# Performance work log

Hardware: AMD Instinct MI355X
Metric: run time of the kernel (lower is better)

The kernel has to match this reference:

```python
import jax, jax.numpy as jnp
import numpy as np

B, N_EX, N_KC, D_E, D_C, D_H = 32, 1024, 128, 64, 64, 64


def setup_inputs() -> dict:
    key = jax.random.key(0)
    ks = jax.random.split(key, 20)
    return {
        "h": jax.random.normal(ks[0], (B, N_KC, D_H), jnp.float32),
        "ex": jax.random.uniform(ks[1], (B, N_EX), jnp.float32),
        "su": jax.random.uniform(ks[2], (B,), jnp.float32),
        "ex_graph": jax.random.uniform(ks[3], (N_EX, N_KC), jnp.float32),
        "kc_gamma": jax.random.normal(ks[4], (N_KC, N_KC), jnp.float32),
        "W_ex": jax.random.normal(ks[5], (D_E, 2 * N_EX), jnp.float32) * 0.02,
        "W_kc": jax.random.normal(ks[6], (D_C, N_KC), jnp.float32) * 0.05,
        "tgru_wih": jax.random.normal(ks[7], (3 * D_H, D_E), jnp.float32) * 0.05,
        "tgru_whh": jax.random.normal(ks[8], (3 * D_H, D_H), jnp.float32) * 0.05,
        "tgru_bih": jax.random.normal(ks[9], (3 * D_H,), jnp.float32) * 0.05,
        "tgru_bhh": jax.random.normal(ks[10], (3 * D_H,), jnp.float32) * 0.05,
        "fpart_w": jax.random.normal(ks[11], (D_H, D_C + D_H), jnp.float32) * 0.05,
        "fpart_b": jax.random.normal(ks[12], (D_H,), jnp.float32) * 0.05,
        "ulin_w": jax.random.normal(ks[13], (D_H, D_H), jnp.float32) * 0.05,
        "ulin_b": jax.random.normal(ks[14], (D_H,), jnp.float32) * 0.05,
        "ugru_wih": jax.random.normal(ks[15], (3 * D_H, D_H), jnp.float32) * 0.05,
        "ugru_whh": jax.random.normal(ks[16], (3 * D_H, D_H), jnp.float32) * 0.05,
        "ugru_bih": jax.random.normal(ks[17], (3 * D_H,), jnp.float32) * 0.05,
        "ugru_bhh": jax.random.normal(ks[18], (3 * D_H,), jnp.float32) * 0.05,
    }


def _gru_cell(x, h, wih, whh, bih, bhh):
    # torch.nn.GRUCell: gates in order r, z, n
    gi = x @ wih.T + bih
    gh = h @ whh.T + bhh
    ir, iz, inn = jnp.split(gi, 3, axis=-1)
    hr, hz, hn = jnp.split(gh, 3, axis=-1)
    r = jax.nn.sigmoid(ir + hr)
    z = jax.nn.sigmoid(iz + hz)
    n = jnp.tanh(inn + r * hn)
    return (1.0 - z) * n + z * h


def reference(h, ex, su, ex_graph, kc_gamma, W_ex, W_kc,
              tgru_wih, tgru_whh, tgru_bih, tgru_bhh,
              fpart_w, fpart_b, ulin_w, ulin_b,
              ugru_wih, ugru_whh, ugru_bih, ugru_bhh):
    bsz, n_kc, d_h = h.shape
    kc_graph = jax.nn.sigmoid(kc_gamma)  # (n_kc, n_kc)

    # exercise embedding from [ex*su, ex*(1-su)]
    x_id = jnp.concatenate([ex * su[:, None], ex * (1.0 - su)[:, None]], axis=-1)  # (B, 2*n_ex)
    x = x_id @ W_ex.T  # (B, d_e)

    kci = ex @ ex_graph  # (B, n_kc)
    kci_flat = kci.reshape(bsz * n_kc, 1)

    # temporal GRU update, gated by kci
    x_rep = jnp.broadcast_to(x[:, None, :], (bsz, n_kc, x.shape[-1])).reshape(bsz * n_kc, -1)
    h_flat = h.reshape(bsz * n_kc, d_h)
    th = _gru_cell(x_rep, h_flat, tgru_wih, tgru_whh, tgru_bih, tgru_bhh)
    new_h = (1.0 - kci_flat) * h_flat + kci_flat * th  # (B*n_kc, d_h)

    delta_h = (new_h - h_flat).reshape(bsz, n_kc, d_h)

    # kc_embeddings(eye(n_kc)) == W_kc.T : (n_kc, d_c)
    e = W_kc.T
    # fpart(concat([delta_h_i, e_j])) split into the two weight blocks
    W_dh = fpart_w[:, :d_h]   # acts on delta_h
    W_e = fpart_w[:, d_h:]    # acts on e
    dpart = delta_h @ W_dh.T                      # (B, n_kc_i, d_h)
    epart = e @ W_e.T + fpart_b                   # (n_kc_j, d_h)
    pre = dpart[:, :, None, :] + epart[None, None, :, :]  # (B, i, j, d_h)
    partij = jax.nn.relu(pre)
    partij = partij * kc_graph[None, :, :, None] * kci[:, :, None, None]
    partj = jnp.sum(partij, axis=1)               # (B, n_kc_j, d_h)

    outj = jax.nn.relu(partj @ ulin_w.T + ulin_b).reshape(bsz * n_kc, d_h)
    kcj = (kci @ kc_graph).reshape(bsz * n_kc, 1)

    uh = _gru_cell(outj, new_h, ugru_wih, ugru_whh, ugru_bih, ugru_bhh)
    h_out = (1.0 - kcj) * new_h + kcj * uh
    return h_out.reshape(bsz, n_kc, d_h)
```

## Files before the change

### kernel.cpp

```cpp
#include <hip/hip_runtime.h>
#include <math.h>

#define NB  32
#define NKC 128
#define DH  64
#define NEX 1024
#define G3  192

#define XOFF    0
#define KCIOFF  2048
#define EPOFF   6144
#define NHOFF   14336
#define DPOFF   276480

__device__ __forceinline__ float sigf(float x) { return 1.0f / (1.0f + expf(-x)); }

__global__ __launch_bounds__(256) void k0_prep(
    const float* __restrict__ ex, const float* __restrict__ su,
    const float* __restrict__ ex_graph, const float* __restrict__ W_ex,
    const float* __restrict__ W_kc, const float* __restrict__ fpart_w,
    const float* __restrict__ fpart_b, float* __restrict__ ws)
{
    int t = threadIdx.x, wave = t >> 6, lane = t & 63;
    int blk = blockIdx.x;
    __shared__ float kred[256];
    __shared__ float fwT[64 * 65];
    __shared__ float wkS[64 * 33];

    if (blk < 256) {
        int b = blk >> 3;
        int dbase = (blk & 7) * 8;
        float sub = su[b];
        const float* exb = ex + (size_t)b * NEX;
        float er[16];
        #pragma unroll
        for (int i = 0; i < 16; ++i) er[i] = exb[lane + i * 64];
        #pragma unroll
        for (int p = 0; p < 2; ++p) {
            int d = dbase + wave * 2 + p;
            const float* wr = W_ex + (size_t)d * (2 * NEX);
            float a1 = 0.f, a2 = 0.f;
            #pragma unroll
            for (int i = 0; i < 16; ++i) {
                int k = lane + i * 64;
                a1 = fmaf(er[i], wr[k], a1);
                a2 = fmaf(er[i], wr[NEX + k], a2);
            }
            float v = sub * a1 + (1.0f - sub) * a2;
            #pragma unroll
            for (int off = 32; off; off >>= 1) v += __shfl_down(v, off, 64);
            if (lane == 0) ws[XOFF + b * DH + d] = v;
        }
    } else if (blk < 512) {
        int q = blk - 256;
        int b = q >> 3, i0 = (q & 7) * 16;
        int i = t & 15, ks = t >> 4;
        const float* exb = ex + (size_t)b * NEX;
        const float* eg = ex_graph + i0 + i;
        int kb = ks * 64;
        float a = 0.f;
        #pragma unroll 4
        for (int k = 0; k < 64; ++k)
            a = fmaf(exb[kb + k], eg[(size_t)(kb + k) * NKC], a);
        kred[t] = a;
        __syncthreads();
        if (t < 16) {
            float s = 0.f;
            #pragma unroll
            for (int r = 0; r < 16; ++r) s += kred[r * 16 + t];
            ws[KCIOFF + b * NKC + i0 + t] = s;
        }
    } else {
        int eb = blk - 512;
        for (int idx = t; idx < 4096; idx += 256) {
            int d = idx >> 6, c = idx & 63;
            fwT[c * 65 + d] = fpart_w[d * 128 + 64 + c];
        }
        for (int idx = t; idx < 2048; idx += 256) {
            int c = idx >> 5, jl = idx & 31;
            wkS[c * 33 + jl] = W_kc[(size_t)c * NKC + eb * 32 + jl];
        }
        __syncthreads();
        float fb = fpart_b[lane];
        #pragma unroll
        for (int q2 = 0; q2 < 8; ++q2) {
            int jl = wave + 4 * q2;
            float a = fb;
            for (int c = 0; c < 64; ++c)
                a = fmaf(wkS[c * 33 + jl], fwT[c * 65 + lane], a);
            ws[EPOFF + (eb * 32 + jl) * DH + lane] = a;
        }
    }
}

__global__ __launch_bounds__(512) void k1_tgru(
    const float* __restrict__ h, const float* __restrict__ tgru_wih,
    const float* __restrict__ tgru_whh, const float* __restrict__ tgru_bih,
    const float* __restrict__ tgru_bhh, const float* __restrict__ fpart_w,
    float* __restrict__ ws)
{
    int t = threadIdx.x, wave = t >> 6, lane = t & 63;
    int b = blockIdx.x >> 3;
    int i0 = (blockIdx.x & 7) * 16;

    __shared__ float whhT[32 * 193];
    __shared__ float wihT[32 * 193];
    __shared__ float ht[16 * DH];
    __shared__ float dlt[16 * DH];
    __shared__ float xs[DH];
    __shared__ float gis[G3];
    __shared__ float bhh3[G3];
    __shared__ float kcis[16];

    const float* hb = h + (size_t)(b * NKC + i0) * DH;
    for (int idx = t; idx < 16 * DH; idx += 512) ht[idx] = hb[idx];
    if (t < DH) xs[t] = ws[XOFF + b * DH + t];
    if (t < G3) bhh3[t] = tgru_bhh[t];
    if (t < 16) kcis[t] = ws[KCIOFF + b * NKC + i0 + t];
    __syncthreads();

    float giA = (t < G3) ? tgru_bih[t] : 0.f;
    float ar[2], az[2], an[2];
    #pragma unroll
    for (int m = 0; m < 2; ++m) {
        ar[m] = bhh3[lane]; az[m] = bhh3[64 + lane]; an[m] = bhh3[128 + lane];
    }

    for (int ch = 0; ch < 2; ++ch) {
        __syncthreads();
        for (int idx = t; idx < G3 * 32; idx += 512) {
            int row = idx >> 5, kk = idx & 31;
            whhT[kk * 193 + row] = tgru_whh[row * DH + ch * 32 + kk];
            wihT[kk * 193 + row] = tgru_wih[row * DH + ch * 32 + kk];
        }
        __syncthreads();
        if (t < G3) {
            for (int kk = 0; kk < 32; ++kk)
                giA = fmaf(wihT[kk * 193 + t], xs[ch * 32 + kk], giA);
        }
        for (int kk = 0; kk < 32; ++kk) {
            float wr = whhT[kk * 193 + lane];
            float wz = whhT[kk * 193 + 64 + lane];
            float wn = whhT[kk * 193 + 128 + lane];
            int k = ch * 32 + kk;
            #pragma unroll
            for (int m = 0; m < 2; ++m) {
                float hk = ht[(wave * 2 + m) * DH + k];
                ar[m] = fmaf(wr, hk, ar[m]);
                az[m] = fmaf(wz, hk, az[m]);
                an[m] = fmaf(wn, hk, an[m]);
            }
        }
    }
    if (t < G3) gis[t] = giA;
    __syncthreads();
    #pragma unroll
    for (int m = 0; m < 2; ++m) {
        int il = wave * 2 + m;
        float hval = ht[il * DH + lane];
        float r = sigf(gis[lane] + ar[m]);
        float z = sigf(gis[64 + lane] + az[m]);
        float n = tanhf(gis[128 + lane] + r * an[m]);
        float th = (1.0f - z) * n + z * hval;
        float kv = kcis[il];
        float nh = (1.0f - kv) * hval + kv * th;
        ws[NHOFF + (size_t)(b * NKC + i0 + il) * DH + lane] = nh;
        dlt[il * DH + lane] = kv * (th - hval);
    }
    __syncthreads();
    for (int idx = t; idx < 4096; idx += 512) {
        int d = idx >> 6, k = idx & 63;
        whhT[k * 65 + d] = fpart_w[d * 128 + k];
    }
    __syncthreads();
    float acc[2];
    acc[0] = 0.f; acc[1] = 0.f;
    for (int k = 0; k < 64; ++k) {
        float w = whhT[k * 65 + lane];
        #pragma unroll
        for (int m = 0; m < 2; ++m)
            acc[m] = fmaf(dlt[(wave * 2 + m) * DH + k], w, acc[m]);
    }
    #pragma unroll
    for (int m = 0; m < 2; ++m)
        ws[DPOFF + (size_t)(b * NKC + i0 + wave * 2 + m) * DH + lane] = acc[m];
}

__global__ __launch_bounds__(512) void kB_update(
    const float* __restrict__ kc_gamma,
    const float* __restrict__ ulin_w, const float* __restrict__ ulin_b,
    const float* __restrict__ ugru_wih, const float* __restrict__ ugru_whh,
    const float* __restrict__ ugru_bih, const float* __restrict__ ugru_bhh,
    float* __restrict__ ws, float* __restrict__ out)
{
    int t = threadIdx.x, wave = t >> 6, lane = t & 63;
    int b = blockIdx.x >> 3;
    int j0 = (blockIdx.x & 7) * 16;

    __shared__ float scratch[12352];
    __shared__ float pjS[16 * DH];
    __shared__ float outjS[16 * DH];
    __shared__ float newhS[16 * DH];
    __shared__ float kcis[NKC];
    __shared__ float kcjS[16];
    __shared__ float bihS[G3];
    __shared__ float bhhS[G3];

    float* dpartS = scratch;
    float* wjS    = scratch + 8192;
    float* epS    = scratch + 10240;

    const float* dp = ws + DPOFF + (size_t)b * NKC * DH;
    for (int idx = t; idx < NKC * DH; idx += 512) dpartS[idx] = dp[idx];
    if (t < NKC) kcis[t] = ws[KCIOFF + b * NKC + t];
    for (int idx = t; idx < 16 * DH; idx += 512) {
        epS[idx]   = ws[EPOFF + j0 * DH + idx];
        newhS[idx] = ws[NHOFF + (size_t)(b * NKC + j0) * DH + idx];
    }
    if (t < G3) { bihS[t] = ugru_bih[t]; bhhS[t] = ugru_bhh[t]; }
    __syncthreads();
    for (int idx = t; idx < 2048; idx += 512) {
        int i = idx >> 4, jl = idx & 15;
        wjS[idx] = kcis[i] * sigf(kc_gamma[i * NKC + j0 + jl]);
    }
    __syncthreads();
    if (t < 16) {
        float s = 0.f;
        for (int i = 0; i < NKC; ++i) s += wjS[i * 16 + t];
        kcjS[t] = s;
    }
    float ep[2], pa[2];
    #pragma unroll
    for (int m = 0; m < 2; ++m) { ep[m] = epS[(wave * 2 + m) * DH + lane]; pa[m] = 0.f; }
    for (int i = 0; i < NKC; ++i) {
        float dv = dpartS[i * DH + lane];
        #pragma unroll
        for (int m = 0; m < 2; ++m) {
            float pre = fmaxf(dv + ep[m], 0.f);
            pa[m] = fmaf(pre, wjS[i * 16 + wave * 2 + m], pa[m]);
        }
    }
    #pragma unroll
    for (int m = 0; m < 2; ++m) pjS[(wave * 2 + m) * DH + lane] = pa[m];
    __syncthreads();
    float* ulT = scratch;
    for (int idx = t; idx < 4096; idx += 512) {
        int d2 = idx >> 6, k = idx & 63;
        ulT[k * 65 + d2] = ulin_w[d2 * DH + k];
    }
    float ulb = ulin_b[lane];
    __syncthreads();
    #pragma unroll
    for (int m = 0; m < 2; ++m) {
        int jl = wave * 2 + m;
        float a = ulb;
        for (int k = 0; k < DH; ++k) a = fmaf(pjS[jl * DH + k], ulT[k * 65 + lane], a);
        outjS[jl * DH + lane] = fmaxf(a, 0.f);
    }
    float* wihT = scratch;
    float* whhT = scratch + 6176;
    float gir[2], giz[2], gin[2], ghr[2], ghz[2], ghn[2];
    #pragma unroll
    for (int m = 0; m < 2; ++m) { gir[m] = giz[m] = gin[m] = ghr[m] = ghz[m] = ghn[m] = 0.f; }
    for (int ch = 0; ch < 2; ++ch) {
        __syncthreads();
        for (int idx = t; idx < G3 * 32; idx += 512) {
            int row = idx >> 5, kk = idx & 31;
            wihT[kk * 193 + row] = ugru_wih[row * DH + ch * 32 + kk];
            whhT[kk * 193 + row] = ugru_whh[row * DH + ch * 32 + kk];
        }
        __syncthreads();
        for (int kk = 0; kk < 32; ++kk) {
            float wir = wihT[kk * 193 + lane];
            float wiz = wihT[kk * 193 + 64 + lane];
            float win = wihT[kk * 193 + 128 + lane];
            float wwr = whhT[kk * 193 + lane];
            float wwz = whhT[kk * 193 + 64 + lane];
            float wwn = whhT[kk * 193 + 128 + lane];
            int k = ch * 32 + kk;
            #pragma unroll
            for (int m = 0; m < 2; ++m) {
                int jl = wave * 2 + m;
                float ov = outjS[jl * DH + k];
                float nv = newhS[jl * DH + k];
                gir[m] = fmaf(wir, ov, gir[m]);
                giz[m] = fmaf(wiz, ov, giz[m]);
                gin[m] = fmaf(win, ov, gin[m]);
                ghr[m] = fmaf(wwr, nv, ghr[m]);
                ghz[m] = fmaf(wwz, nv, ghz[m]);
                ghn[m] = fmaf(wwn, nv, ghn[m]);
            }
        }
    }
    #pragma unroll
    for (int m = 0; m < 2; ++m) {
        int jl = wave * 2 + m;
        float r = sigf(gir[m] + bihS[lane] + ghr[m] + bhhS[lane]);
        float z = sigf(giz[m] + bihS[64 + lane] + ghz[m] + bhhS[64 + lane]);
        float n = tanhf(gin[m] + bihS[128 + lane] + r * (ghn[m] + bhhS[128 + lane]));
        float nh = newhS[jl * DH + lane];
        float uh = (1.0f - z) * n + z * nh;
        float kj = kcjS[jl];
        out[(size_t)(b * NKC + j0 + jl) * DH + lane] = (1.0f - kj) * nh + kj * uh;
    }
}

extern "C" void kernel_launch(void* const* d_in, const int* in_sizes, int n_in,
                              void* d_out, int out_size, void* d_ws, size_t ws_size,
                              hipStream_t stream) {
    const float* h        = (const float*)d_in[0];
    const float* ex       = (const float*)d_in[1];
    const float* su       = (const float*)d_in[2];
    const float* ex_graph = (const float*)d_in[3];
    const float* kc_gamma = (const float*)d_in[4];
    const float* W_ex     = (const float*)d_in[5];
    const float* W_kc     = (const float*)d_in[6];
    const float* tgru_wih = (const float*)d_in[7];
    const float* tgru_whh = (const float*)d_in[8];
    const float* tgru_bih = (const float*)d_in[9];
    const float* tgru_bhh = (const float*)d_in[10];
    const float* fpart_w  = (const float*)d_in[11];
    const float* fpart_b  = (const float*)d_in[12];
    const float* ulin_w   = (const float*)d_in[13];
    const float* ulin_b   = (const float*)d_in[14];
    const float* ugru_wih = (const float*)d_in[15];
    const float* ugru_whh = (const float*)d_in[16];
    const float* ugru_bih = (const float*)d_in[17];
    const float* ugru_bhh = (const float*)d_in[18];
    float* ws  = (float*)d_ws;
    float* out = (float*)d_out;

    hipLaunchKernelGGL(k0_prep, dim3(516), dim3(256), 0, stream,
                       ex, su, ex_graph, W_ex, W_kc, fpart_w, fpart_b, ws);
    hipLaunchKernelGGL(k1_tgru, dim3(256), dim3(512), 0, stream,
                       h, tgru_wih, tgru_whh, tgru_bih, tgru_bhh, fpart_w, ws);
    hipLaunchKernelGGL(kB_update, dim3(256), dim3(512), 0, stream,
                       kc_gamma, ulin_w, ulin_b,
                       ugru_wih, ugru_whh, ugru_bih, ugru_bhh, ws, out);
}
```

Measured before the change: 150.4 us.

## Fuse three kernels into one cooperative kernel with grid syncs

Merges the prep, transfer-GRU and update kernels into a single cooperative launch of 256 blocks that separates the phases with grid.sync. The per-block epart slice and new_h stay in shared memory instead of going through the workspace, and kci is kept locally. This removes two kernel launches and some global round trips. In exchange it adds grid-wide barrier cost and a larger LDS footprint per block, which the cooperative launch needs to stay co-resident.

```diff
diff --git a/kernel.cpp b/kernel.cpp
--- a/kernel.cpp
+++ b/kernel.cpp
@@ -1,5 +1,8 @@
 #include <hip/hip_runtime.h>
+#include <hip/hip_cooperative_groups.h>
 #include <math.h>
+
+namespace cg = cooperative_groups;
 
 #define NB  32
 #define NKC 128
@@ -9,299 +12,276 @@
 
 #define XOFF    0
 #define KCIOFF  2048
-#define EPOFF   6144
-#define NHOFF   14336
-#define DPOFF   276480
+#define DPOFF   6144
 
 __device__ __forceinline__ float sigf(float x) { return 1.0f / (1.0f + expf(-x)); }
 
-__global__ __launch_bounds__(256) void k0_prep(
-    const float* __restrict__ ex, const float* __restrict__ su,
-    const float* __restrict__ ex_graph, const float* __restrict__ W_ex,
-    const float* __restrict__ W_kc, const float* __restrict__ fpart_w,
-    const float* __restrict__ fpart_b, float* __restrict__ ws)
-{
-    int t = threadIdx.x, wave = t >> 6, lane = t & 63;
-    int blk = blockIdx.x;
-    __shared__ float kred[256];
-    __shared__ float fwT[64 * 65];
-    __shared__ float wkS[64 * 33];
-
-    if (blk < 256) {
-        int b = blk >> 3;
-        int dbase = (blk & 7) * 8;
-        float sub = su[b];
-        const float* exb = ex + (size_t)b * NEX;
-        float er[16];
-        #pragma unroll
-        for (int i = 0; i < 16; ++i) er[i] = exb[lane + i * 64];
-        #pragma unroll
-        for (int p = 0; p < 2; ++p) {
-            int d = dbase + wave * 2 + p;
-            const float* wr = W_ex + (size_t)d * (2 * NEX);
-            float a1 = 0.f, a2 = 0.f;
-            #pragma unroll
-            for (int i = 0; i < 16; ++i) {
-                int k = lane + i * 64;
-                a1 = fmaf(er[i], wr[k], a1);
-                a2 = fmaf(er[i], wr[NEX + k], a2);
-            }
-            float v = sub * a1 + (1.0f - sub) * a2;
-            #pragma unroll
-            for (int off = 32; off; off >>= 1) v += __shfl_down(v, off, 64);
-            if (lane == 0) ws[XOFF + b * DH + d] = v;
-        }
-    } else if (blk < 512) {
-        int q = blk - 256;
-        int b = q >> 3, i0 = (q & 7) * 16;
-        int i = t & 15, ks = t >> 4;
-        const float* exb = ex + (size_t)b * NEX;
-        const float* eg = ex_graph + i0 + i;
-        int kb = ks * 64;
-        float a = 0.f;
-        #pragma unroll 4
-        for (int k = 0; k < 64; ++k)
-            a = fmaf(exb[kb + k], eg[(size_t)(kb + k) * NKC], a);
-        kred[t] = a;
-        __syncthreads();
-        if (t < 16) {
-            float s = 0.f;
-            #pragma unroll
-            for (int r = 0; r < 16; ++r) s += kred[r * 16 + t];
-            ws[KCIOFF + b * NKC + i0 + t] = s;
-        }
-    } else {
-        int eb = blk - 512;
-        for (int idx = t; idx < 4096; idx += 256) {
-            int d = idx >> 6, c = idx & 63;
-            fwT[c * 65 + d] = fpart_w[d * 128 + 64 + c];
-        }
-        for (int idx = t; idx < 2048; idx += 256) {
-            int c = idx >> 5, jl = idx & 31;
-            wkS[c * 33 + jl] = W_kc[(size_t)c * NKC + eb * 32 + jl];
-        }
-        __syncthreads();
-        float fb = fpart_b[lane];
-        #pragma unroll
-        for (int q2 = 0; q2 < 8; ++q2) {
-            int jl = wave + 4 * q2;
-            float a = fb;
-            for (int c = 0; c < 64; ++c)
-                a = fmaf(wkS[c * 33 + jl], fwT[c * 65 + lane], a);
-            ws[EPOFF + (eb * 32 + jl) * DH + lane] = a;
-        }
-    }
-}
-
-__global__ __launch_bounds__(512) void k1_tgru(
-    const float* __restrict__ h, const float* __restrict__ tgru_wih,
+__global__ __launch_bounds__(512) void fused_skt(
+    const float* __restrict__ h, const float* __restrict__ ex,
+    const float* __restrict__ su, const float* __restrict__ ex_graph,
+    const float* __restrict__ kc_gamma, const float* __restrict__ W_ex,
+    const float* __restrict__ W_kc, const float* __restrict__ tgru_wih,
     const float* __restrict__ tgru_whh, const float* __restrict__ tgru_bih,
     const float* __restrict__ tgru_bhh, const float* __restrict__ fpart_w,
-    float* __restrict__ ws)
+    const float* __restrict__ fpart_b, const float* __restrict__ ulin_w,
+    const float* __restrict__ ulin_b, const float* __restrict__ ugru_wih,
+    const float* __restrict__ ugru_whh, const float* __restrict__ ugru_bih,
+    const float* __restrict__ ugru_bhh, float* __restrict__ ws,
+    float* __restrict__ out)
 {
+    cg::grid_group grid = cg::this_grid();
     int t = threadIdx.x, wave = t >> 6, lane = t & 63;
     int b = blockIdx.x >> 3;
     int i0 = (blockIdx.x & 7) * 16;
 
-    __shared__ float whhT[32 * 193];
-    __shared__ float wihT[32 * 193];
-    __shared__ float ht[16 * DH];
-    __shared__ float dlt[16 * DH];
+    __shared__ float scratch[12352];
+    __shared__ float pjS[1024];
+    __shared__ float outjS[1024];
+    __shared__ float newhS[1024];
+    __shared__ float epS[1024];
+    __shared__ float ht[1024];
+    __shared__ float dlt[1024];
     __shared__ float xs[DH];
     __shared__ float gis[G3];
     __shared__ float bhh3[G3];
-    __shared__ float kcis[16];
-
-    const float* hb = h + (size_t)(b * NKC + i0) * DH;
-    for (int idx = t; idx < 16 * DH; idx += 512) ht[idx] = hb[idx];
-    if (t < DH) xs[t] = ws[XOFF + b * DH + t];
-    if (t < G3) bhh3[t] = tgru_bhh[t];
-    if (t < 16) kcis[t] = ws[KCIOFF + b * NKC + i0 + t];
-    __syncthreads();
-
-    float giA = (t < G3) ? tgru_bih[t] : 0.f;
-    float ar[2], az[2], an[2];
-    #pragma unroll
-    for (int m = 0; m < 2; ++m) {
-        ar[m] = bhh3[lane]; az[m] = bhh3[64 + lane]; an[m] = bhh3[128 + lane];
-    }
-
-    for (int ch = 0; ch < 2; ++ch) {
-        __syncthreads();
-        for (int idx = t; idx < G3 * 32; idx += 512) {
-            int row = idx >> 5, kk = idx & 31;
-            whhT[kk * 193 + row] = tgru_whh[row * DH + ch * 32 + kk];
-            wihT[kk * 193 + row] = tgru_wih[row * DH + ch * 32 + kk];
-        }
-        __syncthreads();
-        if (t < G3) {
-            for (int kk = 0; kk < 32; ++kk)
-                giA = fmaf(wihT[kk * 193 + t], xs[ch * 32 + kk], giA);
-        }
-        for (int kk = 0; kk < 32; ++kk) {
-            float wr = whhT[kk * 193 + lane];
-            float wz = whhT[kk * 193 + 64 + lane];
-            float wn = whhT[kk * 193 + 128 + lane];
-            int k = ch * 32 + kk;
-            #pragma unroll
-            for (int m = 0; m < 2; ++m) {
-                float hk = ht[(wave * 2 + m) * DH + k];
-                ar[m] = fmaf(wr, hk, ar[m]);
-                az[m] = fmaf(wz, hk, az[m]);
-                an[m] = fmaf(wn, hk, an[m]);
-            }
-        }
-    }
-    if (t < G3) gis[t] = giA;
-    __syncthreads();
-    #pragma unroll
-    for (int m = 0; m < 2; ++m) {
-        int il = wave * 2 + m;
-        float hval = ht[il * DH + lane];
-        float r = sigf(gis[lane] + ar[m]);
-        float z = sigf(gis[64 + lane] + az[m]);
-        float n = tanhf(gis[128 + lane] + r * an[m]);
-        float th = (1.0f - z) * n + z * hval;
-        float kv = kcis[il];
-        float nh = (1.0f - kv) * hval + kv * th;
-        ws[NHOFF + (size_t)(b * NKC + i0 + il) * DH + lane] = nh;
-        dlt[il * DH + lane] = kv * (th - hval);
-    }
-    __syncthreads();
-    for (int idx = t; idx < 4096; idx += 512) {
-        int d = idx >> 6, k = idx & 63;
-        whhT[k * 65 + d] = fpart_w[d * 128 + k];
-    }
-    __syncthreads();
-    float acc[2];
-    acc[0] = 0.f; acc[1] = 0.f;
-    for (int k = 0; k < 64; ++k) {
-        float w = whhT[k * 65 + lane];
-        #pragma unroll
-        for (int m = 0; m < 2; ++m)
-            acc[m] = fmaf(dlt[(wave * 2 + m) * DH + k], w, acc[m]);
-    }
-    #pragma unroll
-    for (int m = 0; m < 2; ++m)
-        ws[DPOFF + (size_t)(b * NKC + i0 + wave * 2 + m) * DH + lane] = acc[m];
-}
-
-__global__ __launch_bounds__(512) void kB_update(
-    const float* __restrict__ kc_gamma,
-    const float* __restrict__ ulin_w, const float* __restrict__ ulin_b,
-    const float* __restrict__ ugru_wih, const float* __restrict__ ugru_whh,
-    const float* __restrict__ ugru_bih, const float* __restrict__ ugru_bhh,
-    float* __restrict__ ws, float* __restrict__ out)
-{
-    int t = threadIdx.x, wave = t >> 6, lane = t & 63;
-    int b = blockIdx.x >> 3;
-    int j0 = (blockIdx.x & 7) * 16;
-
-    __shared__ float scratch[12352];
-    __shared__ float pjS[16 * DH];
-    __shared__ float outjS[16 * DH];
-    __shared__ float newhS[16 * DH];
-    __shared__ float kcis[NKC];
-    __shared__ float kcjS[16];
     __shared__ float bihS[G3];
     __shared__ float bhhS[G3];
-
-    float* dpartS = scratch;
-    float* wjS    = scratch + 8192;
-    float* epS    = scratch + 10240;
-
-    const float* dp = ws + DPOFF + (size_t)b * NKC * DH;
-    for (int idx = t; idx < NKC * DH; idx += 512) dpartS[idx] = dp[idx];
-    if (t < NKC) kcis[t] = ws[KCIOFF + b * NKC + t];
-    for (int idx = t; idx < 16 * DH; idx += 512) {
-        epS[idx]   = ws[EPOFF + j0 * DH + idx];
-        newhS[idx] = ws[NHOFF + (size_t)(b * NKC + j0) * DH + idx];
+    __shared__ float kciL[16];
+    __shared__ float kciF[NKC];
+    __shared__ float kcjS[16];
+
+    {
+        float* exs  = scratch;
+        float* kred = scratch + 1024;
+        float* fwT  = scratch + 2048;
+        float* wkS  = scratch + 6208;
+        *(float2*)&exs[t * 2] = *(const float2*)&ex[(size_t)b * NEX + t * 2];
+        for (int idx = t; idx < 4096; idx += 512) {
+            int d = idx >> 6, c = idx & 63;
+            fwT[c * 65 + d] = fpart_w[d * 128 + 64 + c];
+        }
+        for (int idx = t; idx < 1024; idx += 512) {
+            int c = idx >> 4, jl = idx & 15;
+            wkS[c * 17 + jl] = W_kc[(size_t)c * NKC + i0 + jl];
+        }
+        __syncthreads();
+        {
+            float sub = su[b];
+            int d = (blockIdx.x & 7) * 8 + wave;
+            const float* wr = W_ex + (size_t)d * (2 * NEX);
+            float a1 = 0.f, a2 = 0.f;
+            #pragma unroll
+            for (int i = 0; i < 16; ++i) {
+                int k = lane + i * 64;
+                float e = exs[k];
+                a1 = fmaf(e, wr[k], a1);
+                a2 = fmaf(e, wr[NEX + k], a2);
+            }
+            float v = sub * a1 + (1.0f - sub) * a2;
+            #pragma unroll
+            for (int off = 32; off; off >>= 1) v += __shfl_down(v, off, 64);
+            if (lane == 0) ws[XOFF + b * DH + d] = v;
+        }
+        {
+            int i = t & 15, ks = t >> 4, kb = ks * 32;
+            const float* eg = ex_graph + i0 + i;
+            float a = 0.f;
+            #pragma unroll 4
+            for (int k = 0; k < 32; ++k)
+                a = fmaf(exs[kb + k], eg[(size_t)(kb + k) * NKC], a);
+            kred[t] = a;
+        }
+        #pragma unroll
+        for (int r = 0; r < 2; ++r) {
+            int idx = t + r * 512;
+            int jl = idx >> 6, d = idx & 63;
+            float a = fpart_b[d];
+            for (int c = 0; c < 64; ++c)
+                a = fmaf(wkS[c * 17 + jl], fwT[c * 65 + d], a);
+            epS[jl * DH + d] = a;
+        }
+        __syncthreads();
+        if (t < 16) {
+            float s = 0.f;
+            #pragma unroll
+            for (int r = 0; r < 32; ++r) s += kred[r * 16 + t];
+            kciL[t] = s;
+            ws[KCIOFF + b * NKC + i0 + t] = s;
+        }
     }
-    if (t < G3) { bihS[t] = ugru_bih[t]; bhhS[t] = ugru_bhh[t]; }
-    __syncthreads();
-    for (int idx = t; idx < 2048; idx += 512) {
-        int i = idx >> 4, jl = idx & 15;
-        wjS[idx] = kcis[i] * sigf(kc_gamma[i * NKC + j0 + jl]);
+    grid.sync();
+
+    {
+        float* wihT = scratch;
+        float* whhT = scratch + 6176;
+        if (t < DH) xs[t] = ws[XOFF + b * DH + t];
+        if (t < G3) bhh3[t] = tgru_bhh[t];
+        const float* hb = h + (size_t)(b * NKC + i0) * DH;
+        for (int idx = t; idx < 1024; idx += 512) ht[idx] = hb[idx];
+        __syncthreads();
+
+        float giA = (t < G3) ? tgru_bih[t] : 0.f;
+        float ar[2], az[2], an[2];
+        #pragma unroll
+        for (int m = 0; m < 2; ++m) {
+            ar[m] = bhh3[lane]; az[m] = bhh3[64 + lane]; an[m] = bhh3[128 + lane];
+        }
+        for (int ch = 0; ch < 2; ++ch) {
+            __syncthreads();
+            for (int idx = t; idx < G3 * 32; idx += 512) {
+                int row = idx >> 5, kk = idx & 31;
+                whhT[kk * 193 + row] = tgru_whh[row * DH + ch * 32 + kk];
+                wihT[kk * 193 + row] = tgru_wih[row * DH + ch * 32 + kk];
+            }
+            __syncthreads();
+            if (t < G3) {
+                for (int kk = 0; kk < 32; ++kk)
+                    giA = fmaf(wihT[kk * 193 + t], xs[ch * 32 + kk], giA);
+            }
+            for (int kk = 0; kk < 32; ++kk) {
+                float wr = whhT[kk * 193 + lane];
+                float wz = whhT[kk * 193 + 64 + lane];
+                float wn = whhT[kk * 193 + 128 + lane];
+                int k = ch * 32 + kk;
+                #pragma unroll
+                for (int m = 0; m < 2; ++m) {
+                    float hk = ht[(wave * 2 + m) * DH + k];
+                    ar[m] = fmaf(wr, hk, ar[m]);
+                    az[m] = fmaf(wz, hk, az[m]);
+                    an[m] = fmaf(wn, hk, an[m]);
+                }
+            }
+        }
+        if (t < G3) gis[t] = giA;
+        __syncthreads();
+        #pragma unroll
+        for (int m = 0; m < 2; ++m) {
+            int il = wave * 2 + m;
+            float hval = ht[il * DH + lane];
+            float r = sigf(gis[lane] + ar[m]);
+            float z = sigf(gis[64 + lane] + az[m]);
+            float n = tanhf(gis[128 + lane] + r * an[m]);
+            float th = (1.0f - z) * n + z * hval;
+            float kv = kciL[il];
+            float nh = (1.0f - kv) * hval + kv * th;
+            newhS[il * DH + lane] = nh;
+            dlt[il * DH + lane] = kv * (th - hval);
+        }
+        __syncthreads();
+        for (int idx = t; idx < 4096; idx += 512) {
+            int d = idx >> 6, k = idx & 63;
+            wihT[k * 65 + d] = fpart_w[d * 128 + k];
+        }
+        __syncthreads();
+        float acc[2] = {0.f, 0.f};
+        for (int k = 0; k < 64; ++k) {
+            float w = wihT[k * 65 + lane];
+            #pragma unroll
+            for (int m = 0; m < 2; ++m)
+                acc[m] = fmaf(dlt[(wave * 2 + m) * DH + k], w, acc[m]);
+        }
+        #pragma unroll
+        for (int m = 0; m < 2; ++m)
+            ws[DPOFF + (size_t)(b * NKC + i0 + wave * 2 + m) * DH + lane] = acc[m];
     }
-    __syncthreads();
-    if (t < 16) {
-        float s = 0.f;
-        for (int i = 0; i < NKC; ++i) s += wjS[i * 16 + t];
-        kcjS[t] = s;
-    }
-    float ep[2], pa[2];
-    #pragma unroll
-    for (int m = 0; m < 2; ++m) { ep[m] = epS[(wave * 2 + m) * DH + lane]; pa[m] = 0.f; }
-    for (int i = 0; i < NKC; ++i) {
-        float dv = dpartS[i * DH + lane];
-        #pragma unroll
-        for (int m = 0; m < 2; ++m) {
-            float pre = fmaxf(dv + ep[m], 0.f);
-            pa[m] = fmaf(pre, wjS[i * 16 + wave * 2 + m], pa[m]);
-        }
-    }
-    #pragma unroll
-    for (int m = 0; m < 2; ++m) pjS[(wave * 2 + m) * DH + lane] = pa[m];
-    __syncthreads();
-    float* ulT = scratch;
-    for (int idx = t; idx < 4096; idx += 512) {
-        int d2 = idx >> 6, k = idx & 63;
-        ulT[k * 65 + d2] = ulin_w[d2 * DH + k];
-    }
-    float ulb = ulin_b[lane];
-    __syncthreads();
-    #pragma unroll
-    for (int m = 0; m < 2; ++m) {
-        int jl = wave * 2 + m;
-        float a = ulb;
-        for (int k = 0; k < DH; ++k) a = fmaf(pjS[jl * DH + k], ulT[k * 65 + lane], a);
-        outjS[jl * DH + lane] = fmaxf(a, 0.f);
-    }
-    float* wihT = scratch;
-    float* whhT = scratch + 6176;
-    float gir[2], giz[2], gin[2], ghr[2], ghz[2], ghn[2];
-    #pragma unroll
-    for (int m = 0; m < 2; ++m) { gir[m] = giz[m] = gin[m] = ghr[m] = ghz[m] = ghn[m] = 0.f; }
-    for (int ch = 0; ch < 2; ++ch) {
-        __syncthreads();
-        for (int idx = t; idx < G3 * 32; idx += 512) {
-            int row = idx >> 5, kk = idx & 31;
-            wihT[kk * 193 + row] = ugru_wih[row * DH + ch * 32 + kk];
-            whhT[kk * 193 + row] = ugru_whh[row * DH + ch * 32 + kk];
-        }
-        __syncthreads();
-        for (int kk = 0; kk < 32; ++kk) {
-            float wir = wihT[kk * 193 + lane];
-            float wiz = wihT[kk * 193 + 64 + lane];
-            float win = wihT[kk * 193 + 128 + lane];
-            float wwr = whhT[kk * 193 + lane];
-            float wwz = whhT[kk * 193 + 64 + lane];
-            float wwn = whhT[kk * 193 + 128 + lane];
-            int k = ch * 32 + kk;
+    grid.sync();
+
+    {
+        float* dpartS = scratch;
+        float* wjS    = scratch + 8192;
+        const float* dp = ws + DPOFF + (size_t)b * NKC * DH;
+        for (int idx = t; idx < NKC * DH; idx += 512) dpartS[idx] = dp[idx];
+        if (t < NKC) kciF[t] = ws[KCIOFF + b * NKC + t];
+        if (t < G3) { bihS[t] = ugru_bih[t]; bhhS[t] = ugru_bhh[t]; }
+        __syncthreads();
+        for (int idx = t; idx < 2048; idx += 512) {
+            int i = idx >> 4, jl = idx & 15;
+            wjS[idx] = kciF[i] * sigf(kc_gamma[i * NKC + i0 + jl]);
+        }
+        __syncthreads();
+        if (t < 16) {
+            float s = 0.f;
+            for (int i = 0; i < NKC; ++i) s += wjS[i * 16 + t];
+            kcjS[t] = s;
+        }
+        float ep[2], pa[2];
+        #pragma unroll
+        for (int m = 0; m < 2; ++m) {
+            ep[m] = epS[(wave * 2 + m) * DH + lane]; pa[m] = 0.f;
+        }
+        for (int i = 0; i < NKC; ++i) {
+            float dv = dpartS[i * DH + lane];
             #pragma unroll
             for (int m = 0; m < 2; ++m) {
-                int jl = wave * 2 + m;
-                float ov = outjS[jl * DH + k];
-                float nv = newhS[jl * DH + k];
-                gir[m] = fmaf(wir, ov, gir[m]);
-                giz[m] = fmaf(wiz, ov, giz[m]);
-                gin[m] = fmaf(win, ov, gin[m]);
-                ghr[m] = fmaf(wwr, nv, ghr[m]);
-                ghz[m] = fmaf(wwz, nv, ghz[m]);
-                ghn[m] = fmaf(wwn, nv, ghn[m]);
-            }
-        }
-    }
-    #pragma unroll
-    for (int m = 0; m < 2; ++m) {
-        int jl = wave * 2 + m;
-        float r = sigf(gir[m] + bihS[lane] + ghr[m] + bhhS[lane]);
-        float z = sigf(giz[m] + bihS[64 + lane] + ghz[m] + bhhS[64 + lane]);
-        float n = tanhf(gin[m] + bihS[128 + lane] + r * (ghn[m] + bhhS[128 + lane]));
-        float nh = newhS[jl * DH + lane];
-        float uh = (1.0f - z) * n + z * nh;
-        float kj = kcjS[jl];
-        out[(size_t)(b * NKC + j0 + jl) * DH + lane] = (1.0f - kj) * nh + kj * uh;
+                float pre = fmaxf(dv + ep[m], 0.f);
+                pa[m] = fmaf(pre, wjS[i * 16 + wave * 2 + m], pa[m]);
+            }
+        }
+        #pragma unroll
+        for (int m = 0; m < 2; ++m) pjS[(wave * 2 + m) * DH + lane] = pa[m];
+        __syncthreads();
+        float* ulT = scratch;
+        for (int idx = t; idx < 4096; idx += 512) {
+            int d2 = idx >> 6, k = idx & 63;
+            ulT[k * 65 + d2] = ulin_w[d2 * DH + k];
+        }
+        float ulb = ulin_b[lane];
+        __syncthreads();
+        #pragma unroll
+        for (int m = 0; m < 2; ++m) {
+            int jl = wave * 2 + m;
+            float a = ulb;
+            for (int k = 0; k < DH; ++k)
+                a = fmaf(pjS[jl * DH + k], ulT[k * 65 + lane], a);
+            outjS[jl * DH + lane] = fmaxf(a, 0.f);
+        }
+        float* wihT = scratch;
+        float* whhT = scratch + 6176;
+        float gir[2], giz[2], gin[2], ghr[2], ghz[2], ghn[2];
+        #pragma unroll
+        for (int m = 0; m < 2; ++m)
+            gir[m] = giz[m] = gin[m] = ghr[m] = ghz[m] = ghn[m] = 0.f;
+        for (int ch = 0; ch < 2; ++ch) {
+            __syncthreads();
+            for (int idx = t; idx < G3 * 32; idx += 512) {
+                int row = idx >> 5, kk = idx & 31;
+                wihT[kk * 193 + row] = ugru_wih[row * DH + ch * 32 + kk];
+                whhT[kk * 193 + row] = ugru_whh[row * DH + ch * 32 + kk];
+            }
+            __syncthreads();
+            for (int kk = 0; kk < 32; ++kk) {
+                float wir = wihT[kk * 193 + lane];
+                float wiz = wihT[kk * 193 + 64 + lane];
+                float win = wihT[kk * 193 + 128 + lane];
+                float wwr = whhT[kk * 193 + lane];
+                float wwz = whhT[kk * 193 + 64 + lane];
+                float wwn = whhT[kk * 193 + 128 + lane];
+                int k = ch * 32 + kk;
+                #pragma unroll
+                for (int m = 0; m < 2; ++m) {
+                    int jl = wave * 2 + m;
+                    float ov = outjS[jl * DH + k];
+                    float nv = newhS[jl * DH + k];
+                    gir[m] = fmaf(wir, ov, gir[m]);
+                    giz[m] = fmaf(wiz, ov, giz[m]);
+                    gin[m] = fmaf(win, ov, gin[m]);
+                    ghr[m] = fmaf(wwr, nv, ghr[m]);
+                    ghz[m] = fmaf(wwz, nv, ghz[m]);
+                    ghn[m] = fmaf(wwn, nv, ghn[m]);
+                }
+            }
+        }
+        #pragma unroll
+        for (int m = 0; m < 2; ++m) {
+            int jl = wave * 2 + m;
+            float r = sigf(gir[m] + bihS[lane] + ghr[m] + bhhS[lane]);
+            float z = sigf(giz[m] + bihS[64 + lane] + ghz[m] + bhhS[64 + lane]);
+            float n = tanhf(gin[m] + bihS[128 + lane] + r * (ghn[m] + bhhS[128 + lane]));
+            float nh = newhS[jl * DH + lane];
+            float uh = (1.0f - z) * n + z * nh;
+            float kj = kcjS[jl];
+            out[(size_t)(b * NKC + i0 + jl) * DH + lane] = (1.0f - kj) * nh + kj * uh;
+        }
     }
 }
 
@@ -330,11 +310,13 @@
     float* ws  = (float*)d_ws;
     float* out = (float*)d_out;
 
-    hipLaunchKernelGGL(k0_prep, dim3(516), dim3(256), 0, stream,
-                       ex, su, ex_graph, W_ex, W_kc, fpart_w, fpart_b, ws);
-    hipLaunchKernelGGL(k1_tgru, dim3(256), dim3(512), 0, stream,
-                       h, tgru_wih, tgru_whh, tgru_bih, tgru_bhh, fpart_w, ws);
-    hipLaunchKernelGGL(kB_update, dim3(256), dim3(512), 0, stream,
-                       kc_gamma, ulin_w, ulin_b,
-                       ugru_wih, ugru_whh, ugru_bih, ugru_bhh, ws, out);
+    void* args[] = {
+        (void*)&h, (void*)&ex, (void*)&su, (void*)&ex_graph, (void*)&kc_gamma,
+        (void*)&W_ex, (void*)&W_kc, (void*)&tgru_wih, (void*)&tgru_whh,
+        (void*)&tgru_bih, (void*)&tgru_bhh, (void*)&fpart_w, (void*)&fpart_b,
+        (void*)&ulin_w, (void*)&ulin_b, (void*)&ugru_wih, (void*)&ugru_whh,
+        (void*)&ugru_bih, (void*)&ugru_bhh, (void*)&ws, (void*)&out
+    };
+    hipLaunchCooperativeKernel((void*)fused_skt, dim3(256), dim3(512),
+                               args, 0, stream);
 }
```

Result: slower. 214.6 us (+42.7%).
